# Optimization experiments

Hardware: AMD Instinct MI355X
Metric: run time of the kernel (lower is better)

The kernel has to match this reference:

```python
import jax, jax.numpy as jnp
import numpy as np

EMB = 128
EDGE = 32
STEPS = 3


def _lrelu(x):
    return jax.nn.leaky_relu(x, negative_slope=0.01)


def setup_inputs() -> dict:
    key = jax.random.key(0)
    ks = jax.random.split(key, 16)
    N, E, G = 50000, 400000, 256
    x = jax.random.normal(ks[0], (N, EMB), jnp.float32)
    edge_attr = jax.random.normal(ks[1], (E, EDGE), jnp.float32)
    edge_index = jax.random.randint(ks[2], (2, E), 0, N, jnp.int64)
    batch_ind = jnp.sort(jax.random.randint(ks[3], (N,), 0, G, jnp.int64))
    data_lens = jax.random.randint(ks[4], (G,), 0, G, jnp.int64)
    s = 1.0 / np.sqrt(EMB)
    Wm = jax.random.normal(ks[5], (STEPS, EMB + EDGE, EMB), jnp.float32) * s
    bm = jnp.zeros((STEPS, EMB), jnp.float32)
    Wa = jax.random.normal(ks[6], (STEPS, 3 * EMB, EMB), jnp.float32) * s
    ba = jnp.zeros((STEPS, EMB), jnp.float32)
    Wgate = jax.random.normal(ks[7], (STEPS, EMB), jnp.float32) * s
    bgate = jnp.zeros((STEPS,), jnp.float32)
    Wfeat = jax.random.normal(ks[8], (STEPS, EMB, EMB), jnp.float32) * s
    bfeat = jnp.zeros((STEPS, EMB), jnp.float32)
    Wt = jax.random.normal(ks[9], (STEPS, 2 * EMB, EMB), jnp.float32) * s
    bt = jnp.zeros((STEPS, EMB), jnp.float32)
    return {"x": x, "edge_attr": edge_attr, "Wm": Wm, "bm": bm, "Wa": Wa,
            "ba": ba, "Wgate": Wgate, "bgate": bgate, "Wfeat": Wfeat,
            "bfeat": bfeat, "Wt": Wt, "bt": bt, "edge_index": edge_index,
            "batch_ind": batch_ind, "num_graphs": 256, "data_lens": data_lens}


def reference(x, edge_attr, Wm, bm, Wa, ba, Wgate, bgate, Wfeat, bfeat, Wt, bt,
              edge_index, batch_ind, num_graphs, data_lens):
    N = x.shape[0]
    src, dst = edge_index[0], edge_index[1]  # PyG: x_j = x[src], aggregate at dst
    xg = jnp.zeros((num_graphs, EMB), x.dtype)  # xg_init is None -> zeros
    for s in range(STEPS):
        # GraphNet: gather -> message MLP -> scatter-max -> update MLP + residual
        xg_node = xg[batch_ind]                                   # [N, emb]
        z = jnp.concatenate([x[src], edge_attr], axis=1)          # [E, emb+edge]
        m = _lrelu(z @ Wm[s] + bm[s])                             # [E, emb]
        agg = jax.ops.segment_max(m, dst, num_segments=N)         # [N, emb]
        agg = jnp.where(jnp.isneginf(agg), 0.0, agg)              # PyG fills empty with 0
        z2 = jnp.concatenate([x, xg_node, agg], axis=1)           # [N, 3*emb]
        x = _lrelu(z2 @ Wa[s] + ba[s]) + x
        # GlobalNode: segment-softmax attention pooling + transform + residual
        gate = x @ Wgate[s] + bgate[s]                            # [N]
        gmax = jax.ops.segment_max(gate, batch_ind, num_segments=num_graphs)
        gmax = jnp.where(jnp.isneginf(gmax), 0.0, gmax)
        e = jnp.exp(gate - gmax[batch_ind])
        denom = jax.ops.segment_sum(e, batch_ind, num_segments=num_graphs)
        alpha = e / denom[batch_ind]                              # [N]
        feat = _lrelu(x @ Wfeat[s] + bfeat[s])                    # [N, emb]
        pooled = jax.ops.segment_sum(alpha[:, None] * feat, batch_ind,
                                     num_segments=num_graphs)     # [G, emb]
        cat = jnp.concatenate([pooled, xg], axis=1)               # [G, 2*emb]
        xg = _lrelu(cat @ Wt[s] + bt[s]) + xg
    return x, xg
```

## Files before the change

kernel.cpp:

```cpp
#include <hip/hip_runtime.h>
#include <hip/hip_bf16.h>

#define EMB 128
#define EDGE 32
#define STEPS 3
#define DSTRIDE 16

typedef short bf8s __attribute__((ext_vector_type(8)));
typedef float f32x4 __attribute__((ext_vector_type(4)));

__device__ __forceinline__ float lrelu(float v) { return v > 0.0f ? v : 0.01f * v; }
__device__ __forceinline__ unsigned short f2bf(float f) {
    unsigned u = __float_as_uint(f);
    u += 0x7fffu + ((u >> 16) & 1u);
    return (unsigned short)(u >> 16);
}
__device__ __forceinline__ float bf2f(unsigned short s) {
    return __uint_as_float(((unsigned)s) << 16);
}
__device__ __forceinline__ unsigned pk2bf(float x, float y) {
    __hip_bfloat162 h = __float22bfloat162_rn(make_float2(x, y));
    return *(unsigned*)&h;
}

__global__ void k_hist(const int* __restrict__ dst, int E, int* __restrict__ deg) {
    int e = blockIdx.x * 256 + threadIdx.x;
    if (e < E) atomicAdd(&deg[dst[e]], 1);
}

__global__ void k_scan1(const int* __restrict__ deg, int N, int* __restrict__ rowptr,
                        int* __restrict__ bsums) {
    __shared__ int s[256];
    int t = threadIdx.x;
    int i = blockIdx.x * 256 + t;
    int v = (i < N) ? deg[i] : 0;
    s[t] = v;
    __syncthreads();
#pragma unroll
    for (int off = 1; off < 256; off <<= 1) {
        int x = (t >= off) ? s[t - off] : 0;
        __syncthreads();
        s[t] += x;
        __syncthreads();
    }
    if (i < N) rowptr[i] = s[t] - v;
    if (t == 255) bsums[blockIdx.x] = s[255];
}

__global__ void k_scan2(int* __restrict__ bsums, int NB) {
    __shared__ int s[256];
    __shared__ int carry;
    int t = threadIdx.x;
    if (t == 0) carry = 0;
    __syncthreads();
    for (int base = 0; base < NB; base += 256) {
        int i = base + t;
        int v = (i < NB) ? bsums[i] : 0;
        s[t] = v;
        __syncthreads();
#pragma unroll
        for (int off = 1; off < 256; off <<= 1) {
            int x = (t >= off) ? s[t - off] : 0;
            __syncthreads();
            s[t] += x;
            __syncthreads();
        }
        int excl = s[t] - v + carry;
        if (i < NB) bsums[i] = excl;
        int tot = s[255];
        __syncthreads();
        if (t == 0) carry += tot;
        __syncthreads();
    }
}

__global__ void k_scan3(int* __restrict__ rowptr, const int* __restrict__ bsums,
                        int* __restrict__ cursor, int N, int E) {
    int i = blockIdx.x * 256 + threadIdx.x;
    if (i < N) {
        int v = rowptr[i] + bsums[i >> 8];
        rowptr[i] = v;
        cursor[i] = v;
    }
    if (i == 0) rowptr[N] = E;
}

__global__ void k_fill(const int* __restrict__ src, const int* __restrict__ dst, int E,
                       int* __restrict__ cursor, int2* __restrict__ sp2) {
    int e = blockIdx.x * 256 + threadIdx.x;
    if (e >= E) return;
    int d = dst[e];
    int p = atomicAdd(&cursor[d], 1);
    sp2[p] = make_int2(src[e], e);
}

__global__ __launch_bounds__(256) void k_eaperm(const float* __restrict__ ea,
                                                const int2* __restrict__ sp2,
                                                unsigned short* __restrict__ ea16p,
                                                int* __restrict__ srcp, int E) {
    int p = blockIdx.x * 256 + threadIdx.x;
    if (p >= E) return;
    int2 sp = sp2[p];
    srcp[p] = sp.x;
    const float4* er = (const float4*)(ea + (size_t)sp.y * EDGE);
    union { unsigned u[16]; int4 v[4]; } o;
#pragma unroll
    for (int q = 0; q < 8; ++q) {
        float4 v = er[q];
        o.u[2 * q]     = pk2bf(v.x, v.y);
        o.u[2 * q + 1] = pk2bf(v.z, v.w);
    }
    int4* dp = (int4*)(ea16p + (size_t)p * EDGE);
#pragma unroll
    for (int q = 0; q < 4; ++q) dp[q] = o.v[q];
}

__global__ __launch_bounds__(256) void k_setup(const float* __restrict__ x0,
                                               unsigned short* __restrict__ x16,
                                               int N, int XB, int NB,
                                               const float* __restrict__ ba,
                                               float* __restrict__ gb,
                                               float* __restrict__ xg_a,
                                               const int* __restrict__ batch,
                                               int* __restrict__ gstart, int G,
                                               unsigned short* __restrict__ h16,
                                               int* __restrict__ deg,
                                               float* __restrict__ denom) {
    int b = blockIdx.x, t = threadIdx.x;
    if (b < XB) {
        size_t idx = ((size_t)b * 256 + t) * 8;
        if (idx < (size_t)N * EMB) {
            const float4* s = (const float4*)(x0 + idx);
            float4 v0 = s[0], v1 = s[1];
            union { bf8s v; unsigned u[4]; } o;
            o.u[0] = pk2bf(v0.x, v0.y);
            o.u[1] = pk2bf(v0.z, v0.w);
            o.u[2] = pk2bf(v1.x, v1.y);
            o.u[3] = pk2bf(v1.z, v1.w);
            *(bf8s*)(x16 + idx) = o.v;
        }
        return;
    }
    b -= XB;
    if (b < NB) {
        int i = b * 256 + t;
        if (i < N) deg[i] = 0;
        return;
    }
    b -= NB;
    if (b < G) {
        if (t < EMB) gb[(size_t)b * EMB + t] = ba[t];
        else xg_a[(size_t)b * EMB + (t - EMB)] = 0.f;
        if (t == 0) {
            denom[(size_t)b * DSTRIDE] = 0.f;
            int lo = 0, hi = N;
            while (lo < hi) {
                int mid = (lo + hi) >> 1;
                if (batch[mid] < b) lo = mid + 1; else hi = mid;
            }
            gstart[b] = lo;
        }
        return;
    }
    if (t < EMB) h16[(size_t)N * EMB + t] = 0xFF80u;
    if (t == EMB) gstart[G] = N;
}

__global__ __launch_bounds__(256) void k_wpack(const float* __restrict__ Wm,
                                               const float* __restrict__ Wa,
                                               const float* __restrict__ Wfeat,
                                               unsigned short* __restrict__ wpack) {
    int gid = blockIdx.x * 256 + threadIdx.x;
    int unit = gid >> 14;
    int e = gid & 16383;
    int s = unit / 5, u = unit % 5;
    const float* src; int rows;
    switch (u) {
        case 0: src = Wm + (size_t)s * 160 * EMB;             rows = 128; break;
        case 1: src = Wm + (size_t)s * 160 * EMB + 128 * EMB; rows = 32;  break;
        case 2: src = Wa + (size_t)s * 384 * EMB;             rows = 128; break;
        case 3: src = Wa + (size_t)s * 384 * EMB + 256 * EMB; rows = 128; break;
        default: src = Wfeat + (size_t)s * EMB * EMB;         rows = 128; break;
    }
    int k = e >> 7, n = e & 127;
    if (k >= rows) return;
    unsigned short b = f2bf(src[(size_t)k * EMB + n]);
    int kc = k >> 5, c = n >> 4, lane = (n & 15) | (((k & 31) >> 3) << 4), j = k & 7;
    wpack[(size_t)unit * 16384 + ((size_t)(kc * 8 + c) * 64 + lane) * 8 + j] = b;
}

__device__ __forceinline__ void loadAa(const unsigned short* __restrict__ A16, int row0,
                                       int wv, int lane, int N, bf8s af[4]) {
    int li = lane & 15, oct = lane >> 4;
    int m = row0 + wv * 16 + li;
    if (m >= N) m = N - 1;
    const bf8s* ar = (const bf8s*)(A16 + (size_t)m * EMB);
#pragma unroll
    for (int kc = 0; kc < 4; ++kc) af[kc] = ar[kc * 4 + oct];
}
__device__ __forceinline__ void stageB(const unsigned short* __restrict__ Bp,
                                       unsigned short* lB, int tid) {
#pragma unroll
    for (int i = 0; i < 8; ++i) {
        int idx = tid + i * 256;
        ((int4*)lB)[idx] = ((const int4*)Bp)[idx];
    }
}
__device__ __forceinline__ void mfma128r(const bf8s af[4], const unsigned short* lB,
                                         f32x4 acc[8], int lane) {
#pragma unroll
    for (int kc = 0; kc < 4; ++kc) {
#pragma unroll
        for (int c = 0; c < 8; ++c) {
            bf8s b = *(const bf8s*)&lB[((kc * 8 + c) * 64 + lane) * 8];
            acc[c] = __builtin_amdgcn_mfma_f32_16x16x32_bf16(af[kc], b, acc[c], 0, 0, 0);
        }
    }
}

__device__ __forceinline__ void bias_epi(const f32x4 acc[8], int row0, int wv, int lane,
                                         const float* __restrict__ bias,
                                         unsigned short* __restrict__ C, int N) {
    int li = lane & 15, quad = lane >> 4;
    float bcol[8];
#pragma unroll
    for (int c = 0; c < 8; ++c) bcol[c] = bias[c * 16 + li];
#pragma unroll
    for (int rr = 0; rr < 4; ++rr) {
        int m = row0 + wv * 16 + quad * 4 + rr;
        if (m < N) {
            union { bf8s v; unsigned u[4]; } o;
#pragma unroll
            for (int j = 0; j < 4; ++j)
                o.u[j] = pk2bf(acc[2 * j][rr] + bcol[2 * j],
                               acc[2 * j + 1][rr] + bcol[2 * j + 1]);
            *(bf8s*)&C[(size_t)m * EMB + li * 8] = o.v;
        }
    }
}

__global__ __launch_bounds__(256) void k_gemm_bias(const unsigned short* __restrict__ A16,
                                                   const unsigned short* __restrict__ Bp,
                                                   const float* __restrict__ bias,
                                                   unsigned short* __restrict__ C, int N) {
    __shared__ unsigned short lB[16384];
    int tid = threadIdx.x, wv = tid >> 6, lane = tid & 63;
    int row0 = blockIdx.x * 64;
    stageB(Bp, lB, tid);
    bf8s af[4];
    loadAa(A16, row0, wv, lane, N, af);
    __syncthreads();
    f32x4 acc[8];
#pragma unroll
    for (int c = 0; c < 8; ++c) acc[c] = (f32x4){0.f, 0.f, 0.f, 0.f};
    mfma128r(af, lB, acc, lane);
    bias_epi(acc, row0, wv, lane, bias, C, N);
}

__global__ __launch_bounds__(256) void k_gemm_node(unsigned short* __restrict__ x16,
                                                   const unsigned short* __restrict__ agg16,
                                                   const unsigned short* __restrict__ BpX,
                                                   const unsigned short* __restrict__ BpA,
                                                   const float* __restrict__ gb,
                                                   const int* __restrict__ batch,
                                                   float* __restrict__ xout_f32,
                                                   const float* __restrict__ wg,
                                                   const float* __restrict__ bg,
                                                   float* __restrict__ egate,
                                                   float* __restrict__ denom,
                                                   float* __restrict__ pooled, int G, int N) {
    __shared__ unsigned short lB[16384];
    int tid = threadIdx.x, wv = tid >> 6, lane = tid & 63;
    int row0 = blockIdx.x * 64;
    if (blockIdx.x < (unsigned)G && tid < EMB)
        pooled[(size_t)blockIdx.x * EMB + tid] = 0.f;
    stageB(BpX, lB, tid);
    bf8s af[4];
    loadAa(x16, row0, wv, lane, N, af);
    __syncthreads();
    f32x4 acc[8];
#pragma unroll
    for (int c = 0; c < 8; ++c) acc[c] = (f32x4){0.f, 0.f, 0.f, 0.f};
    mfma128r(af, lB, acc, lane);
    __syncthreads();
    stageB(BpA, lB, tid);
    loadAa(agg16, row0, wv, lane, N, af);
    __syncthreads();
    mfma128r(af, lB, acc, lane);
    int li = lane & 15, quad = lane >> 4;
    float gpart[4] = {0.f, 0.f, 0.f, 0.f};
#pragma unroll
    for (int c = 0; c < 8; ++c) {
        int col = c * 16 + li;
        float wgc = wg[col];
#pragma unroll
        for (int rr = 0; rr < 4; ++rr) {
            int m = row0 + wv * 16 + quad * 4 + rr;
            if (m < N) {
                int g = batch[m];
                float b = gb[(size_t)g * EMB + col];
                float res = bf2f(x16[(size_t)m * EMB + col]);
                float v = lrelu(acc[c][rr] + b) + res;
                x16[(size_t)m * EMB + col] = f2bf(v);
                if (xout_f32) xout_f32[(size_t)m * EMB + col] = v;
                gpart[rr] = fmaf(v, wgc, gpart[rr]);
            }
        }
    }
#pragma unroll
    for (int rr = 0; rr < 4; ++rr) {
#pragma unroll
        for (int off = 1; off < 16; off <<= 1)
            gpart[rr] += __shfl_xor(gpart[rr], off, 64);
    }
    float b0 = bg[0];
    int rb = row0 + wv * 16;
    float ge[4];
    float sq = 0.f;
#pragma unroll
    for (int rr = 0; rr < 4; ++rr) {
        int m = rb + quad * 4 + rr;
        float g = (m < N) ? __expf(gpart[rr] + b0) : 0.f;
        ge[rr] = g;
        sq += g;
    }
    if (li == 0) {
#pragma unroll
        for (int rr = 0; rr < 4; ++rr) {
            int m = rb + quad * 4 + rr;
            if (m < N) egate[m] = ge[rr];
        }
    }
    float wsum = sq;
    wsum += __shfl_xor(wsum, 16, 64);
    wsum += __shfl_xor(wsum, 32, 64);
    if (rb < N) {
        int mlast = rb + 15; if (mlast >= N) mlast = N - 1;
        if (batch[rb] == batch[mlast]) {
            if (lane == 0) atomicAdd(&denom[(size_t)batch[rb] * DSTRIDE], wsum);
        } else if (li == 0) {
#pragma unroll
            for (int rr = 0; rr < 4; ++rr) {
                int m = rb + quad * 4 + rr;
                if (m < N) atomicAdd(&denom[(size_t)batch[m] * DSTRIDE], ge[rr]);
            }
        }
    }
}

__device__ __forceinline__ void feat_epi(const f32x4 acc[8], int row0, int wv, int lane,
                                         const float* __restrict__ bias,
                                         const float* __restrict__ egate,
                                         const float* __restrict__ denom,
                                         const int* __restrict__ batch,
                                         float* __restrict__ pooled, int N) {
    int li = lane & 15, quad = lane >> 4;
    int rb = row0 + wv * 16;
    if (rb >= N) return;
    float alpha[4];
    int grow[4];
#pragma unroll
    for (int rr = 0; rr < 4; ++rr) {
        int m = rb + quad * 4 + rr;
        if (m < N) {
            int g = batch[m];
            grow[rr] = g;
            alpha[rr] = egate[m] / denom[(size_t)g * DSTRIDE];
        } else { alpha[rr] = 0.f; grow[rr] = 0; }
    }
    int gs = batch[rb];
    int mlast = rb + 15; if (mlast >= N) mlast = N - 1;
    bool uni = (gs == batch[mlast]);
#pragma unroll
    for (int c = 0; c < 8; ++c) {
        int col = c * 16 + li;
        float b = bias[col];
        float v0 = alpha[0] * lrelu(acc[c][0] + b);
        float v1 = alpha[1] * lrelu(acc[c][1] + b);
        float v2 = alpha[2] * lrelu(acc[c][2] + b);
        float v3 = alpha[3] * lrelu(acc[c][3] + b);
        if (uni) {
            float s = (v0 + v1) + (v2 + v3);
            s += __shfl_xor(s, 16, 64);
            s += __shfl_xor(s, 32, 64);
            if (quad == 0) atomicAdd(&pooled[(size_t)gs * EMB + col], s);
        } else {
            if (rb + quad * 4 + 0 < N) atomicAdd(&pooled[(size_t)grow[0] * EMB + col], v0);
            if (rb + quad * 4 + 1 < N) atomicAdd(&pooled[(size_t)grow[1] * EMB + col], v1);
            if (rb + quad * 4 + 2 < N) atomicAdd(&pooled[(size_t)grow[2] * EMB + col], v2);
            if (rb + quad * 4 + 3 < N) atomicAdd(&pooled[(size_t)grow[3] * EMB + col], v3);
        }
    }
}

__global__ __launch_bounds__(256) void k_gemm_feat(const unsigned short* __restrict__ A16,
                                                   const unsigned short* __restrict__ Bp,
                                                   const float* __restrict__ bias,
                                                   const float* __restrict__ egate,
                                                   const float* __restrict__ denom,
                                                   const int* __restrict__ batch,
                                                   float* __restrict__ pooled, int N) {
    __shared__ unsigned short lB[16384];
    int tid = threadIdx.x, wv = tid >> 6, lane = tid & 63;
    int row0 = blockIdx.x * 64;
    stageB(Bp, lB, tid);
    bf8s af[4];
    loadAa(A16, row0, wv, lane, N, af);
    __syncthreads();
    f32x4 acc[8];
#pragma unroll
    for (int c = 0; c < 8; ++c) acc[c] = (f32x4){0.f, 0.f, 0.f, 0.f};
    mfma128r(af, lB, acc, lane);
    feat_epi(acc, row0, wv, lane, bias, egate, denom, batch, pooled, N);
}

__global__ __launch_bounds__(256) void k_gemm_fb(const unsigned short* __restrict__ A16,
                                                 const unsigned short* __restrict__ BpF,
                                                 const float* __restrict__ bfeat_s,
                                                 const float* __restrict__ egate,
                                                 const float* __restrict__ denom,
                                                 const int* __restrict__ batch,
                                                 float* __restrict__ pooled,
                                                 const unsigned short* __restrict__ BpBn,
                                                 const float* __restrict__ bm_next,
                                                 unsigned short* __restrict__ h16, int N) {
    __shared__ unsigned short lB[16384];
    int tid = threadIdx.x, wv = tid >> 6, lane = tid & 63;
    int row0 = blockIdx.x * 64;
    stageB(BpF, lB, tid);
    bf8s af[4];
    loadAa(A16, row0, wv, lane, N, af);
    __syncthreads();
    f32x4 accF[8], accB[8];
#pragma unroll
    for (int c = 0; c < 8; ++c) {
        accF[c] = (f32x4){0.f, 0.f, 0.f, 0.f};
        accB[c] = (f32x4){0.f, 0.f, 0.f, 0.f};
    }
    mfma128r(af, lB, accF, lane);
    __syncthreads();
    stageB(BpBn, lB, tid);
    __syncthreads();
    mfma128r(af, lB, accB, lane);
    feat_epi(accF, row0, wv, lane, bfeat_s, egate, denom, batch, pooled, N);
    bias_epi(accB, row0, wv, lane, bm_next, h16, N);
}

__global__ __launch_bounds__(128) void k_xg(const float* __restrict__ pooled,
                                            const float* __restrict__ xg,
                                            const float* __restrict__ Wt,
                                            const float* __restrict__ bt,
                                            float* __restrict__ xg_out,
                                            const float* __restrict__ WaGn,
                                            const float* __restrict__ ban,
                                            float* __restrict__ gb,
                                            float* __restrict__ denom) {
    int g = blockIdx.x, c = threadIdx.x;
    __shared__ float row[256];
    row[c] = pooled[(size_t)g * EMB + c];
    row[c + 128] = xg[(size_t)g * EMB + c];
    __syncthreads();
    if (c == 0) denom[(size_t)g * DSTRIDE] = 0.f;
    float acc = bt[c];
#pragma unroll 8
    for (int k = 0; k < 256; ++k) acc = fmaf(row[k], Wt[(size_t)k * EMB + c], acc);
    float v = lrelu(acc) + row[c + 128];
    xg_out[(size_t)g * EMB + c] = v;
    if (WaGn) {
        __syncthreads();
        row[c] = v;
        __syncthreads();
        float a2 = ban[c];
#pragma unroll 8
        for (int k = 0; k < EMB; ++k) a2 = fmaf(row[k], WaGn[(size_t)k * EMB + c], a2);
        gb[(size_t)g * EMB + c] = a2;
    }
}

__global__ __launch_bounds__(256) void k_fagg(const unsigned short* __restrict__ h,
                                              const unsigned short* __restrict__ ea16p,
                                              const int* __restrict__ srcp,
                                              const int* __restrict__ rowptr,
                                              const unsigned short* __restrict__ Bp,
                                              unsigned short* __restrict__ agg, int N) {
    __shared__ unsigned short lB[4096];
    int tid = threadIdx.x;
    ((int4*)lB)[tid]       = ((const int4*)Bp)[tid];
    ((int4*)lB)[tid + 256] = ((const int4*)Bp)[tid + 256];
    __syncthreads();
    int wv = tid >> 6, lane = tid & 63;
    int li = lane & 15, oct = lane >> 4;
    int nA = blockIdx.x * 8 + wv * 2;
    if (nA >= N) return;
    int nB = nA + 1;
    bool hasB = (nB < N);
    int r0 = rowptr[nA];
    int r1 = rowptr[nA + 1];
    int r2 = hasB ? rowptr[nB + 1] : r1;
    int degA = r1 - r0, degB = r2 - r1;

    float vmA[8], vmB[8];
#pragma unroll
    for (int ci = 0; ci < 8; ++ci) { vmA[ci] = -__builtin_inff(); vmB[ci] = -__builtin_inff(); }

    {
        int pA = r0 + li; if (pA >= r1) pA = (r1 > r0) ? r1 - 1 : 0;
        int pB = r1 + li; if (pB >= r2) pB = (r2 > r1) ? r2 - 1 : 0;
        int srcvA = srcp[pA];
        int srcvB = srcp[pB];
        bf8s aA = *(const bf8s*)&ea16p[(size_t)pA * EDGE + oct * 8];
        bf8s aB = *(const bf8s*)&ea16p[(size_t)pB * EDGE + oct * 8];
        union { bf8s v; unsigned short s[8]; } hvA[4], hvB[4];
#pragma unroll
        for (int rr = 0; rr < 4; ++rr) {
            int sr = __shfl(srcvA, oct * 4 + rr, 16);
            if (oct * 4 + rr >= degA) sr = N;
            hvA[rr].v = *(const bf8s*)&h[(size_t)sr * EMB + li * 8];
        }
#pragma unroll
        for (int rr = 0; rr < 4; ++rr) {
            int sr = __shfl(srcvB, oct * 4 + rr, 16);
            if (oct * 4 + rr >= degB) sr = N;
            hvB[rr].v = *(const bf8s*)&h[(size_t)sr * EMB + li * 8];
        }
#pragma unroll
        for (int ci = 0; ci < 8; ++ci) {
            bf8s bb = *(const bf8s*)&lB[(ci * 64 + lane) * 8];
            f32x4 acc;
            acc[0] = bf2f(hvA[0].s[ci]);
            acc[1] = bf2f(hvA[1].s[ci]);
            acc[2] = bf2f(hvA[2].s[ci]);
            acc[3] = bf2f(hvA[3].s[ci]);
            acc = __builtin_amdgcn_mfma_f32_16x16x32_bf16(aA, bb, acc, 0, 0, 0);
#pragma unroll
            for (int rr = 0; rr < 4; ++rr) vmA[ci] = fmaxf(vmA[ci], acc[rr]);
        }
#pragma unroll
        for (int ci = 0; ci < 8; ++ci) {
            bf8s bb = *(const bf8s*)&lB[(ci * 64 + lane) * 8];
            f32x4 acc;
            acc[0] = bf2f(hvB[0].s[ci]);
            acc[1] = bf2f(hvB[1].s[ci]);
            acc[2] = bf2f(hvB[2].s[ci]);
            acc[3] = bf2f(hvB[3].s[ci]);
            acc = __builtin_amdgcn_mfma_f32_16x16x32_bf16(aB, bb, acc, 0, 0, 0);
#pragma unroll
            for (int rr = 0; rr < 4; ++rr) vmB[ci] = fmaxf(vmB[ci], acc[rr]);
        }
    }
    for (int b = 16; b < degA; b += 16) {
        int p = r0 + b + li;
        if (p > r1 - 1) p = r1 - 1;
        int srcv = srcp[p];
        bf8s a = *(const bf8s*)&ea16p[(size_t)p * EDGE + oct * 8];
        union { bf8s v; unsigned short s[8]; } hv[4];
#pragma unroll
        for (int rr = 0; rr < 4; ++rr) {
            int sr = __shfl(srcv, oct * 4 + rr, 16);
            if (b + oct * 4 + rr >= degA) sr = N;
            hv[rr].v = *(const bf8s*)&h[(size_t)sr * EMB + li * 8];
        }
#pragma unroll
        for (int ci = 0; ci < 8; ++ci) {
            bf8s bb = *(const bf8s*)&lB[(ci * 64 + lane) * 8];
            f32x4 acc;
            acc[0] = bf2f(hv[0].s[ci]);
            acc[1] = bf2f(hv[1].s[ci]);
            acc[2] = bf2f(hv[2].s[ci]);
            acc[3] = bf2f(hv[3].s[ci]);
            acc = __builtin_amdgcn_mfma_f32_16x16x32_bf16(a, bb, acc, 0, 0, 0);
#pragma unroll
            for (int rr = 0; rr < 4; ++rr) vmA[ci] = fmaxf(vmA[ci], acc[rr]);
        }
    }
    for (int b = 16; b < degB; b += 16) {
        int p = r1 + b + li;
        if (p > r2 - 1) p = r2 - 1;
        int srcv = srcp[p];
        bf8s a = *(const bf8s*)&ea16p[(size_t)p * EDGE + oct * 8];
        union { bf8s v; unsigned short s[8]; } hv[4];
#pragma unroll
        for (int rr = 0; rr < 4; ++rr) {
            int sr = __shfl(srcv, oct * 4 + rr, 16);
            if (b + oct * 4 + rr >= degB) sr = N;
            hv[rr].v = *(const bf8s*)&h[(size_t)sr * EMB + li * 8];
        }
#pragma unroll
        for (int ci = 0; ci < 8; ++ci) {
            bf8s bb = *(const bf8s*)&lB[(ci * 64 + lane) * 8];
            f32x4 acc;
            acc[0] = bf2f(hv[0].s[ci]);
            acc[1] = bf2f(hv[1].s[ci]);
            acc[2] = bf2f(hv[2].s[ci]);
            acc[3] = bf2f(hv[3].s[ci]);
            acc = __builtin_amdgcn_mfma_f32_16x16x32_bf16(a, bb, acc, 0, 0, 0);
#pragma unroll
            for (int rr = 0; rr < 4; ++rr) vmB[ci] = fmaxf(vmB[ci], acc[rr]);
        }
    }
#pragma unroll
    for (int ci = 0; ci < 8; ++ci) {
        vmA[ci] = fmaxf(vmA[ci], __shfl_xor(vmA[ci], 16, 64));
        vmA[ci] = fmaxf(vmA[ci], __shfl_xor(vmA[ci], 32, 64));
        vmB[ci] = fmaxf(vmB[ci], __shfl_xor(vmB[ci], 16, 64));
        vmB[ci] = fmaxf(vmB[ci], __shfl_xor(vmB[ci], 32, 64));
    }
    {
        float s0 = (oct == 0) ? vmA[0] : (oct == 1) ? vmA[1] : (oct == 2) ? vmA[2] : vmA[3];
        float s1 = (oct == 0) ? vmA[4] : (oct == 1) ? vmA[5] : (oct == 2) ? vmA[6] : vmA[7];
        s0 = lrelu(s0);
        s1 = lrelu(s1);
        if (degA == 0) { s0 = 0.f; s1 = 0.f; }
        agg[(size_t)nA * EMB + oct * 16 + li]       = f2bf(s0);
        agg[(size_t)nA * EMB + (oct + 4) * 16 + li] = f2bf(s1);
    }
    if (hasB) {
        float s0 = (oct == 0) ? vmB[0] : (oct == 1) ? vmB[1] : (oct == 2) ? vmB[2] : vmB[3];
        float s1 = (oct == 0) ? vmB[4] : (oct == 1) ? vmB[5] : (oct == 2) ? vmB[6] : vmB[7];
        s0 = lrelu(s0);
        s1 = lrelu(s1);
        if (degB == 0) { s0 = 0.f; s1 = 0.f; }
        agg[(size_t)nB * EMB + oct * 16 + li]       = f2bf(s0);
        agg[(size_t)nB * EMB + (oct + 4) * 16 + li] = f2bf(s1);
    }
}

extern "C" void kernel_launch(void* const* d_in, const int* in_sizes, int n_in,
                              void* d_out, int out_size, void* d_ws, size_t ws_size,
                              hipStream_t stream) {
    const float* x0    = (const float*)d_in[0];
    const float* ea    = (const float*)d_in[1];
    const float* Wm    = (const float*)d_in[2];
    const float* bm    = (const float*)d_in[3];
    const float* Wa    = (const float*)d_in[4];
    const float* ba    = (const float*)d_in[5];
    const float* Wgate = (const float*)d_in[6];
    const float* bgate = (const float*)d_in[7];
    const float* Wfeat = (const float*)d_in[8];
    const float* bfeat = (const float*)d_in[9];
    const float* Wt    = (const float*)d_in[10];
    const float* bt    = (const float*)d_in[11];
    const int*   eidx  = (const int*)d_in[12];
    const int*   batch = (const int*)d_in[13];

    int N = in_sizes[0] / EMB;
    int E = in_sizes[1] / EDGE;
    int G = in_sizes[15];

    char* w = (char*)d_ws;
    auto alloc = [&](size_t bytes) {
        char* p = w;
        w += (bytes + 255) & ~(size_t)255;
        return p;
    };
    unsigned short* h16   = (unsigned short*)alloc((size_t)(N + 1) * EMB * 2);
    unsigned short* x16   = (unsigned short*)alloc((size_t)N * EMB * 2);
    unsigned short* agg16 = (unsigned short*)alloc((size_t)N * EMB * 2);
    float* egate  = (float*)alloc((size_t)N * 4);
    float* gb     = (float*)alloc((size_t)G * EMB * 4);
    float* pooled = (float*)alloc((size_t)G * EMB * 4);
    float* denom  = (float*)alloc((size_t)G * DSTRIDE * 4);
    float* xg_a   = (float*)alloc((size_t)G * EMB * 4);
    float* xg_b   = (float*)alloc((size_t)G * EMB * 4);
    int* deg      = (int*)alloc((size_t)N * 4);
    int* rowptr   = (int*)alloc((size_t)(N + 1) * 4);
    int* cursor   = (int*)alloc((size_t)N * 4);
    int2* sp2     = (int2*)alloc((size_t)E * 8);
    int* srcp     = (int*)alloc((size_t)E * 4);
    unsigned short* ea16p = (unsigned short*)alloc((size_t)E * EDGE * 2);
    int* gstart   = (int*)alloc((size_t)(G + 1) * 4);
    int* bsums    = (int*)alloc(1024 * 4);
    unsigned short* wpack = (unsigned short*)alloc((size_t)15 * 16384 * 2);

    const int* esrc = eidx;
    const int* edst = eidx + E;
    int ebl = (E + 255) / 256;
    int NB  = (N + 255) / 256;
    int XB  = ((size_t)N * EMB / 8 + 255) / 256;

    k_setup<<<XB + NB + G + 1, 256, 0, stream>>>(x0, x16, N, XB, NB, ba, gb, xg_a,
                                                 batch, gstart, G, h16, deg, denom);
    k_hist<<<ebl, 256, 0, stream>>>(edst, E, deg);
    k_scan1<<<NB, 256, 0, stream>>>(deg, N, rowptr, bsums);
    k_scan2<<<1, 256, 0, stream>>>(bsums, NB);
    k_scan3<<<NB, 256, 0, stream>>>(rowptr, bsums, cursor, N, E);
    k_fill<<<ebl, 256, 0, stream>>>(esrc, edst, E, cursor, sp2);
    k_eaperm<<<ebl, 256, 0, stream>>>(ea, sp2, ea16p, srcp, E);
    k_wpack<<<960, 256, 0, stream>>>(Wm, Wa, Wfeat, wpack);

    int gemm_blocks = (N + 63) / 64;
    int fagg_blocks = (N + 7) / 8;

    float* xg_cur = xg_a;
    float* xg_nxt = xg_b;

    k_gemm_bias<<<gemm_blocks, 256, 0, stream>>>(x16, wpack + 0 * 16384, bm, h16, N);

    for (int s = 0; s < STEPS; ++s) {
        const unsigned short* wp = wpack + (size_t)s * 5 * 16384;
        bool last = (s == STEPS - 1);

        k_fagg<<<fagg_blocks, 256, 0, stream>>>(h16, ea16p, srcp, rowptr, wp + 1 * 16384,
                                                agg16, N);
        k_gemm_node<<<gemm_blocks, 256, 0, stream>>>(x16, agg16, wp + 2 * 16384,
                                                     wp + 3 * 16384, gb, batch,
                                                     last ? (float*)d_out : nullptr,
                                                     Wgate + s * EMB, bgate + s,
                                                     egate, denom, pooled, G, N);
        if (!last) {
            k_gemm_fb<<<gemm_blocks, 256, 0, stream>>>(x16, wp + 4 * 16384, bfeat + s * EMB,
                                                       egate, denom, batch, pooled,
                                                       wp + 5 * 16384 ,
                                                       bm + (s + 1) * EMB, h16, N);
        } else {
            k_gemm_feat<<<gemm_blocks, 256, 0, stream>>>(x16, wp + 4 * 16384,
                                                         bfeat + s * EMB, egate, denom,
                                                         batch, pooled, N);
        }
        const float* WaGn = !last ? Wa + (size_t)(s + 1) * 384 * EMB + 128 * EMB : nullptr;
        const float* ban  = !last ? ba + (s + 1) * EMB : nullptr;
        float* xgout = last ? (float*)d_out + (size_t)N * EMB : xg_nxt;
        k_xg<<<G, 128, 0, stream>>>(pooled, xg_cur, Wt + (size_t)s * 256 * EMB,
                                    bt + s * EMB, xgout, WaGn, ban, gb, denom);

        float* tmp = xg_cur; xg_cur = xg_nxt; xg_nxt = tmp;
    }
}
```

Baseline: 519.0 us.

## Fuse node update, feature pooling and next-step message GEMM into one kernel

```diff
diff --git a/kernel.cpp b/kernel.cpp
--- a/kernel.cpp
+++ b/kernel.cpp
@@ -125,7 +125,8 @@
                                                int* __restrict__ gstart, int G,
                                                unsigned short* __restrict__ h16,
                                                int* __restrict__ deg,
-                                               float* __restrict__ denom) {
+                                               float* __restrict__ denom,
+                                               float* __restrict__ pooled) {
     int b = blockIdx.x, t = threadIdx.x;
     if (b < XB) {
         size_t idx = ((size_t)b * 256 + t) * 8;
@@ -149,8 +150,12 @@
     }
     b -= NB;
     if (b < G) {
-        if (t < EMB) gb[(size_t)b * EMB + t] = ba[t];
-        else xg_a[(size_t)b * EMB + (t - EMB)] = 0.f;
+        if (t < EMB) {
+            gb[(size_t)b * EMB + t] = ba[t];
+            pooled[(size_t)b * EMB + t] = 0.f;
+        } else {
+            xg_a[(size_t)b * EMB + (t - EMB)] = 0.f;
+        }
         if (t == 0) {
             denom[(size_t)b * DSTRIDE] = 0.f;
             int lo = 0, hi = N;
@@ -257,23 +262,27 @@
     bias_epi(acc, row0, wv, lane, bias, C, N);
 }
 
-__global__ __launch_bounds__(256) void k_gemm_node(unsigned short* __restrict__ x16,
-                                                   const unsigned short* __restrict__ agg16,
-                                                   const unsigned short* __restrict__ BpX,
-                                                   const unsigned short* __restrict__ BpA,
-                                                   const float* __restrict__ gb,
-                                                   const int* __restrict__ batch,
-                                                   float* __restrict__ xout_f32,
-                                                   const float* __restrict__ wg,
-                                                   const float* __restrict__ bg,
-                                                   float* __restrict__ egate,
-                                                   float* __restrict__ denom,
-                                                   float* __restrict__ pooled, int G, int N) {
+__global__ __launch_bounds__(256) void k_gemm_nfb(unsigned short* __restrict__ x16,
+                                                  const unsigned short* __restrict__ agg16,
+                                                  const unsigned short* __restrict__ BpX,
+                                                  const unsigned short* __restrict__ BpA,
+                                                  const float* __restrict__ gb,
+                                                  const int* __restrict__ batch,
+                                                  float* __restrict__ xout_f32,
+                                                  const float* __restrict__ wg,
+                                                  const float* __restrict__ bg,
+                                                  float* __restrict__ denom,
+                                                  const unsigned short* __restrict__ BpF,
+                                                  const float* __restrict__ bfeat_s,
+                                                  float* __restrict__ pooled,
+                                                  const unsigned short* __restrict__ BpBn,
+                                                  const float* __restrict__ bm_next,
+                                                  unsigned short* __restrict__ h16, int N) {
     __shared__ unsigned short lB[16384];
     int tid = threadIdx.x, wv = tid >> 6, lane = tid & 63;
     int row0 = blockIdx.x * 64;
-    if (blockIdx.x < (unsigned)G && tid < EMB)
-        pooled[(size_t)blockIdx.x * EMB + tid] = 0.f;
+    int li = lane & 15, quad = lane >> 4;
+
     stageB(BpX, lB, tid);
     bf8s af[4];
     loadAa(x16, row0, wv, lane, N, af);
@@ -287,7 +296,7 @@
     loadAa(agg16, row0, wv, lane, N, af);
     __syncthreads();
     mfma128r(af, lB, acc, lane);
-    int li = lane & 15, quad = lane >> 4;
+
     float gpart[4] = {0.f, 0.f, 0.f, 0.f};
 #pragma unroll
     for (int c = 0; c < 8; ++c) {
@@ -324,20 +333,17 @@
         ge[rr] = g;
         sq += g;
     }
-    if (li == 0) {
-#pragma unroll
-        for (int rr = 0; rr < 4; ++rr) {
-            int m = rb + quad * 4 + rr;
-            if (m < N) egate[m] = ge[rr];
-        }
-    }
     float wsum = sq;
     wsum += __shfl_xor(wsum, 16, 64);
     wsum += __shfl_xor(wsum, 32, 64);
+    int gs = 0, mlast = 0;
+    bool uni = false;
     if (rb < N) {
-        int mlast = rb + 15; if (mlast >= N) mlast = N - 1;
-        if (batch[rb] == batch[mlast]) {
-            if (lane == 0) atomicAdd(&denom[(size_t)batch[rb] * DSTRIDE], wsum);
+        gs = batch[rb];
+        mlast = rb + 15; if (mlast >= N) mlast = N - 1;
+        uni = (gs == batch[mlast]);
+        if (uni) {
+            if (lane == 0) atomicAdd(&denom[(size_t)gs * DSTRIDE], wsum);
         } else if (li == 0) {
 #pragma unroll
             for (int rr = 0; rr < 4; ++rr) {
@@ -346,107 +352,49 @@
             }
         }
     }
-}
-
-__device__ __forceinline__ void feat_epi(const f32x4 acc[8], int row0, int wv, int lane,
-                                         const float* __restrict__ bias,
-                                         const float* __restrict__ egate,
-                                         const float* __restrict__ denom,
-                                         const int* __restrict__ batch,
-                                         float* __restrict__ pooled, int N) {
-    int li = lane & 15, quad = lane >> 4;
-    int rb = row0 + wv * 16;
-    if (rb >= N) return;
-    float alpha[4];
-    int grow[4];
-#pragma unroll
-    for (int rr = 0; rr < 4; ++rr) {
-        int m = rb + quad * 4 + rr;
-        if (m < N) {
-            int g = batch[m];
-            grow[rr] = g;
-            alpha[rr] = egate[m] / denom[(size_t)g * DSTRIDE];
-        } else { alpha[rr] = 0.f; grow[rr] = 0; }
-    }
-    int gs = batch[rb];
-    int mlast = rb + 15; if (mlast >= N) mlast = N - 1;
-    bool uni = (gs == batch[mlast]);
-#pragma unroll
-    for (int c = 0; c < 8; ++c) {
-        int col = c * 16 + li;
-        float b = bias[col];
-        float v0 = alpha[0] * lrelu(acc[c][0] + b);
-        float v1 = alpha[1] * lrelu(acc[c][1] + b);
-        float v2 = alpha[2] * lrelu(acc[c][2] + b);
-        float v3 = alpha[3] * lrelu(acc[c][3] + b);
-        if (uni) {
-            float s = (v0 + v1) + (v2 + v3);
-            s += __shfl_xor(s, 16, 64);
-            s += __shfl_xor(s, 32, 64);
-            if (quad == 0) atomicAdd(&pooled[(size_t)gs * EMB + col], s);
-        } else {
-            if (rb + quad * 4 + 0 < N) atomicAdd(&pooled[(size_t)grow[0] * EMB + col], v0);
-            if (rb + quad * 4 + 1 < N) atomicAdd(&pooled[(size_t)grow[1] * EMB + col], v1);
-            if (rb + quad * 4 + 2 < N) atomicAdd(&pooled[(size_t)grow[2] * EMB + col], v2);
-            if (rb + quad * 4 + 3 < N) atomicAdd(&pooled[(size_t)grow[3] * EMB + col], v3);
-        }
-    }
-}
-
-__global__ __launch_bounds__(256) void k_gemm_feat(const unsigned short* __restrict__ A16,
-                                                   const unsigned short* __restrict__ Bp,
-                                                   const float* __restrict__ bias,
-                                                   const float* __restrict__ egate,
-                                                   const float* __restrict__ denom,
-                                                   const int* __restrict__ batch,
-                                                   float* __restrict__ pooled, int N) {
-    __shared__ unsigned short lB[16384];
-    int tid = threadIdx.x, wv = tid >> 6, lane = tid & 63;
-    int row0 = blockIdx.x * 64;
-    stageB(Bp, lB, tid);
-    bf8s af[4];
-    loadAa(A16, row0, wv, lane, N, af);
-    __syncthreads();
-    f32x4 acc[8];
+
+    __syncthreads();
+    stageB(BpF, lB, tid);
+    loadAa(x16, row0, wv, lane, N, af);
+    __syncthreads();
 #pragma unroll
     for (int c = 0; c < 8; ++c) acc[c] = (f32x4){0.f, 0.f, 0.f, 0.f};
     mfma128r(af, lB, acc, lane);
-    feat_epi(acc, row0, wv, lane, bias, egate, denom, batch, pooled, N);
-}
-
-__global__ __launch_bounds__(256) void k_gemm_fb(const unsigned short* __restrict__ A16,
-                                                 const unsigned short* __restrict__ BpF,
-                                                 const float* __restrict__ bfeat_s,
-                                                 const float* __restrict__ egate,
-                                                 const float* __restrict__ denom,
-                                                 const int* __restrict__ batch,
-                                                 float* __restrict__ pooled,
-                                                 const unsigned short* __restrict__ BpBn,
-                                                 const float* __restrict__ bm_next,
-                                                 unsigned short* __restrict__ h16, int N) {
-    __shared__ unsigned short lB[16384];
-    int tid = threadIdx.x, wv = tid >> 6, lane = tid & 63;
-    int row0 = blockIdx.x * 64;
-    stageB(BpF, lB, tid);
-    bf8s af[4];
-    loadAa(A16, row0, wv, lane, N, af);
-    __syncthreads();
-    f32x4 accF[8], accB[8];
-#pragma unroll
-    for (int c = 0; c < 8; ++c) {
-        accF[c] = (f32x4){0.f, 0.f, 0.f, 0.f};
-        accB[c] = (f32x4){0.f, 0.f, 0.f, 0.f};
-    }
-    mfma128r(af, lB, accF, lane);
-    __syncthreads();
-    stageB(BpBn, lB, tid);
-    __syncthreads();
-    mfma128r(af, lB, accB, lane);
-    feat_epi(accF, row0, wv, lane, bfeat_s, egate, denom, batch, pooled, N);
-    bias_epi(accB, row0, wv, lane, bm_next, h16, N);
-}
-
-__global__ __launch_bounds__(128) void k_xg(const float* __restrict__ pooled,
+    if (rb < N) {
+#pragma unroll
+        for (int c = 0; c < 8; ++c) {
+            int col = c * 16 + li;
+            float b = bfeat_s[col];
+            float v0 = ge[0] * lrelu(acc[c][0] + b);
+            float v1 = ge[1] * lrelu(acc[c][1] + b);
+            float v2 = ge[2] * lrelu(acc[c][2] + b);
+            float v3 = ge[3] * lrelu(acc[c][3] + b);
+            if (uni) {
+                float s = (v0 + v1) + (v2 + v3);
+                s += __shfl_xor(s, 16, 64);
+                s += __shfl_xor(s, 32, 64);
+                if (quad == 0) atomicAdd(&pooled[(size_t)gs * EMB + col], s);
+            } else {
+                if (rb + quad * 4 + 0 < N) atomicAdd(&pooled[(size_t)batch[rb + quad * 4 + 0] * EMB + col], v0);
+                if (rb + quad * 4 + 1 < N) atomicAdd(&pooled[(size_t)batch[rb + quad * 4 + 1] * EMB + col], v1);
+                if (rb + quad * 4 + 2 < N) atomicAdd(&pooled[(size_t)batch[rb + quad * 4 + 2] * EMB + col], v2);
+                if (rb + quad * 4 + 3 < N) atomicAdd(&pooled[(size_t)batch[rb + quad * 4 + 3] * EMB + col], v3);
+            }
+        }
+    }
+
+    if (BpBn) {
+        __syncthreads();
+        stageB(BpBn, lB, tid);
+        __syncthreads();
+#pragma unroll
+        for (int c = 0; c < 8; ++c) acc[c] = (f32x4){0.f, 0.f, 0.f, 0.f};
+        mfma128r(af, lB, acc, lane);
+        bias_epi(acc, row0, wv, lane, bm_next, h16, N);
+    }
+}
+
+__global__ __launch_bounds__(128) void k_xg(float* __restrict__ pooled,
                                             const float* __restrict__ xg,
                                             const float* __restrict__ Wt,
                                             const float* __restrict__ bt,
@@ -457,9 +405,12 @@
                                             float* __restrict__ denom) {
     int g = blockIdx.x, c = threadIdx.x;
     __shared__ float row[256];
-    row[c] = pooled[(size_t)g * EMB + c];
+    float dv = denom[(size_t)g * DSTRIDE];
+    float pr = pooled[(size_t)g * EMB + c];
+    row[c] = (dv > 0.f) ? pr / dv : 0.f;
     row[c + 128] = xg[(size_t)g * EMB + c];
     __syncthreads();
+    pooled[(size_t)g * EMB + c] = 0.f;
     if (c == 0) denom[(size_t)g * DSTRIDE] = 0.f;
     float acc = bt[c];
 #pragma unroll 8
@@ -656,7 +607,6 @@
     unsigned short* h16   = (unsigned short*)alloc((size_t)(N + 1) * EMB * 2);
     unsigned short* x16   = (unsigned short*)alloc((size_t)N * EMB * 2);
     unsigned short* agg16 = (unsigned short*)alloc((size_t)N * EMB * 2);
-    float* egate  = (float*)alloc((size_t)N * 4);
     float* gb     = (float*)alloc((size_t)G * EMB * 4);
     float* pooled = (float*)alloc((size_t)G * EMB * 4);
     float* denom  = (float*)alloc((size_t)G * DSTRIDE * 4);
@@ -679,7 +629,8 @@
     int XB  = ((size_t)N * EMB / 8 + 255) / 256;
 
     k_setup<<<XB + NB + G + 1, 256, 0, stream>>>(x0, x16, N, XB, NB, ba, gb, xg_a,
-                                                 batch, gstart, G, h16, deg, denom);
+                                                 batch, gstart, G, h16, deg, denom,
+                                                 pooled);
     k_hist<<<ebl, 256, 0, stream>>>(edst, E, deg);
     k_scan1<<<NB, 256, 0, stream>>>(deg, N, rowptr, bsums);
     k_scan2<<<1, 256, 0, stream>>>(bsums, NB);
@@ -702,21 +653,12 @@
 
         k_fagg<<<fagg_blocks, 256, 0, stream>>>(h16, ea16p, srcp, rowptr, wp + 1 * 16384,
                                                 agg16, N);
-        k_gemm_node<<<gemm_blocks, 256, 0, stream>>>(x16, agg16, wp + 2 * 16384,
-                                                     wp + 3 * 16384, gb, batch,
-                                                     last ? (float*)d_out : nullptr,
-                                                     Wgate + s * EMB, bgate + s,
-                                                     egate, denom, pooled, G, N);
-        if (!last) {
-            k_gemm_fb<<<gemm_blocks, 256, 0, stream>>>(x16, wp + 4 * 16384, bfeat + s * EMB,
-                                                       egate, denom, batch, pooled,
-                                                       wp + 5 * 16384 ,
-                                                       bm + (s + 1) * EMB, h16, N);
-        } else {
-            k_gemm_feat<<<gemm_blocks, 256, 0, stream>>>(x16, wp + 4 * 16384,
-                                                         bfeat + s * EMB, egate, denom,
-                                                         batch, pooled, N);
-        }
+        k_gemm_nfb<<<gemm_blocks, 256, 0, stream>>>(
+            x16, agg16, wp + 2 * 16384, wp + 3 * 16384, gb, batch,
+            last ? (float*)d_out : nullptr, Wgate + s * EMB, bgate + s, denom,
+            wp + 4 * 16384, bfeat + s * EMB, pooled,
+            last ? nullptr : wp + 5 * 16384, last ? nullptr : bm + (s + 1) * EMB,
+            h16, N);
         const float* WaGn = !last ? Wa + (size_t)(s + 1) * 384 * EMB + 128 * EMB : nullptr;
         const float* ban  = !last ? ba + (s + 1) * EMB : nullptr;
         float* xgout = last ? (float*)d_out + (size_t)N * EMB : xg_nxt;
```

New measurement: 556.9 us. 7.3% more time.
